# Kernel tuning notes

Hardware: AMD Instinct MI355X
Metric: run time of the kernel (lower is better)

## Reference

```python
import jax, jax.numpy as jnp
import numpy as np

EPS = 1e-3  # keras LayerNormalization default epsilon


def _layernorm(y, gamma, beta):
    m = jnp.mean(y, axis=-1, keepdims=True)
    v = jnp.var(y, axis=-1, keepdims=True)
    return (y - m) * jax.lax.rsqrt(v + EPS) * gamma + beta


def setup_inputs() -> dict:
    key = jax.random.key(0)
    ks = jax.random.split(key, 3)
    B, S, D, F = 4, 8192, 512, 2048
    x = jax.random.normal(ks[0], (B, S, D), dtype=jnp.float32)
    W1 = jax.random.normal(ks[1], (D, F), dtype=jnp.float32) * (1.0 / np.sqrt(D))
    b1 = jnp.zeros((F,), dtype=jnp.float32)
    W2 = jax.random.normal(ks[2], (F, D), dtype=jnp.float32) * (1.0 / np.sqrt(F))
    b2 = jnp.zeros((D,), dtype=jnp.float32)
    g1 = jnp.ones((D,), dtype=jnp.float32)
    be1 = jnp.zeros((D,), dtype=jnp.float32)
    g2 = jnp.ones((D,), dtype=jnp.float32)
    be2 = jnp.zeros((D,), dtype=jnp.float32)
    return {"x": x, "W1": W1, "b1": b1, "W2": W2, "b2": b2,
            "g1": g1, "be1": be1, "g2": g2, "be2": be2}


def reference(x, W1, b1, W2, b2, g1, be1, g2, be2):
    # 2D FFT over (seq, embed) axes; keep real part (FNet mixing)
    fft = jnp.real(jnp.fft.fft2(x.astype(jnp.complex64), axes=(-2, -1)))
    proj_input = _layernorm(x + fft, g1, be1)
    # FFN: Dense(dense_dim, relu) -> Dense(embed_dim)
    h = jax.nn.relu(jnp.einsum('bsd,df->bsf', proj_input, W1) + b1)
    proj_output = jnp.einsum('bsf,fd->bsd', h, W2) + b2
    return _layernorm(proj_input + proj_output, g2, be2)
```

## Files before the change

### kernel.cpp

```cpp
#include <hip/hip_runtime.h>

typedef unsigned short u16;
typedef unsigned int u32;
typedef short short8 __attribute__((ext_vector_type(8)));
typedef float f32x4 __attribute__((ext_vector_type(4)));

#define LN_EPS 1e-3f
#define PI2 6.28318530717958647692f
#define AS1 __attribute__((address_space(1)))
#define AS3 __attribute__((address_space(3)))

__device__ __forceinline__ u16 f2bf(float f) {
  u32 u = __float_as_uint(f);
  u += 0x7fffu + ((u >> 16) & 1u);
  return (u16)(u >> 16);
}
__device__ __forceinline__ float bf2f(u16 h) {
  return __uint_as_float(((u32)h) << 16);
}

__global__ __launch_bounds__(256) void prep_w(const float* __restrict__ W,
                                              u16* __restrict__ Wt, int R, int C) {
  __shared__ float tile[32][33];
  const int ct = C >> 5;
  int bc = blockIdx.x % ct;
  int br = blockIdx.x / ct;
  int tx = threadIdx.x & 31, ty = threadIdx.x >> 5;
  int r0 = br << 5, c0 = bc << 5;
#pragma unroll
  for (int i = 0; i < 32; i += 8)
    tile[ty + i][tx] = W[(size_t)(r0 + ty + i) * C + c0 + tx];
  __syncthreads();
#pragma unroll
  for (int i = 0; i < 32; i += 8)
    Wt[(size_t)(c0 + ty + i) * R + r0 + tx] = f2bf(tile[tx][ty + i]);
}

__global__ __launch_bounds__(256) void transpose_x(const float* __restrict__ x,
                                                   u16* __restrict__ xt) {
  __shared__ float tile[32][33];
  int blk = blockIdx.x;
  int b = blk >> 12;
  int rem = blk & 4095;
  int st = rem >> 4;
  int dt = rem & 15;
  int tx = threadIdx.x & 31, ty = threadIdx.x >> 5;
  int s0 = st << 5, d0 = dt << 5;
#pragma unroll
  for (int i = 0; i < 32; i += 8)
    tile[ty + i][tx] = x[(((size_t)(b << 13) + s0 + ty + i) << 9) + d0 + tx];
  __syncthreads();
#pragma unroll
  for (int i = 0; i < 32; i += 8)
    xt[(((size_t)(b << 9) + d0 + ty + i) << 13) + s0 + tx] = f2bf(tile[tx][ty + i]);
}

__device__ __constant__ float C16r[8] = {1.f, 0.92387953f, 0.70710678f, 0.38268343f,
                                         0.f, -0.38268343f, -0.70710678f, -0.92387953f};
__device__ __constant__ float C16i[8] = {0.f, -0.38268343f, -0.70710678f, -0.92387953f,
                                         -1.f, -0.92387953f, -0.70710678f, -0.38268343f};
__device__ __constant__ float C8r[4] = {1.f, 0.70710678f, 0.f, -0.70710678f};
__device__ __constant__ float C8i[4] = {0.f, -0.70710678f, -1.f, -0.70710678f};
__device__ __constant__ float C4r[2] = {1.f, 0.f};
__device__ __constant__ float C4i[2] = {0.f, -1.f};
__device__ __constant__ float C32r[16] = {
    1.f, 0.98078528f, 0.92387953f, 0.83146961f, 0.70710678f, 0.55557023f,
    0.38268343f, 0.19509032f, 0.f, -0.19509032f, -0.38268343f, -0.55557023f,
    -0.70710678f, -0.83146961f, -0.92387953f, -0.98078528f};
__device__ __constant__ float C32i[16] = {
    0.f, -0.19509032f, -0.38268343f, -0.55557023f, -0.70710678f, -0.83146961f,
    -0.92387953f, -0.98078528f, -1.f, -0.98078528f, -0.92387953f, -0.83146961f,
    -0.70710678f, -0.55557023f, -0.38268343f, -0.19509032f};
__device__ __constant__ int REV4[16] = {0, 8, 4, 12, 2, 10, 6, 14,
                                        1, 9, 5, 13, 3, 11, 7, 15};

__device__ __forceinline__ constexpr int rev4c(int v) {
  return ((v & 1) << 3) | ((v & 2) << 1) | ((v & 4) >> 1) | ((v & 8) >> 3);
}

#define BFLY(ar, ai, br, bi, wr, wi)                 \
  {                                                  \
    float dr_ = (ar) - (br), di_ = (ai) - (bi);      \
    (ar) += (br);                                    \
    (ai) += (bi);                                    \
    (br) = dr_ * (wr)-di_ * (wi);                    \
    (bi) = dr_ * (wi) + di_ * (wr);                  \
  }

__global__ __launch_bounds__(512) void fft_s(u16* __restrict__ X, u16* __restrict__ Xim) {
  __shared__ float zr[8448], zi[8448];
  const int t = threadIdx.x;
  const int b = blockIdx.x >> 8;
  const int d0 = (blockIdx.x & 255) << 1;
  u16* r0 = X + (((size_t)(b << 9) + d0) << 13);
  u16* r1 = r0 + 8192;

  float xr[16], xi[16];
#pragma unroll
  for (int e = 0; e < 16; ++e) {
    xr[e] = bf2f(r0[t + (e << 9)]);
    xi[e] = bf2f(r1[t + (e << 9)]);
  }

  float c1, s1;
  sincosf(-PI2 * (float)t * (1.0f / 8192.0f), &s1, &c1);
  float c2 = c1 * c1 - s1 * s1, s2 = 2.f * c1 * s1;
  float c4 = c2 * c2 - s2 * s2, s4 = 2.f * c2 * s2;
  float c8 = c4 * c4 - s4 * s4, s8 = 2.f * c4 * s4;
#pragma unroll
  for (int e = 0; e < 8; ++e) {
    float wr = c1 * C16r[e] - s1 * C16i[e];
    float wi = c1 * C16i[e] + s1 * C16r[e];
    BFLY(xr[e], xi[e], xr[e + 8], xi[e + 8], wr, wi);
  }
#pragma unroll
  for (int e = 0; e < 16; ++e) {
    if ((e & 4) == 0) {
      int eb = e & 3;
      float wr = c2 * C8r[eb] - s2 * C8i[eb];
      float wi = c2 * C8i[eb] + s2 * C8r[eb];
      BFLY(xr[e], xi[e], xr[e + 4], xi[e + 4], wr, wi);
    }
  }
#pragma unroll
  for (int e = 0; e < 16; ++e) {
    if (((e >> 1) & 1) == 0) {
      int eb = e & 1;
      float wr = c4 * C4r[eb] - s4 * C4i[eb];
      float wi = c4 * C4i[eb] + s4 * C4r[eb];
      BFLY(xr[e], xi[e], xr[e + 2], xi[e + 2], wr, wi);
    }
  }
#pragma unroll
  for (int e = 0; e < 16; e += 2) {
    BFLY(xr[e], xi[e], xr[e + 1], xi[e + 1], c8, s8);
  }

#pragma unroll
  for (int e = 0; e < 16; ++e) {
    int idx = t + (e << 9);
    int a = idx + (idx >> 5);
    zr[a] = xr[e];
    zi[a] = xi[e];
  }
  __syncthreads();
  {
    const int f = t >> 5, l = t & 31;
#pragma unroll
    for (int e = 0; e < 16; ++e) {
      int idx = (f << 9) + (e << 5) + l;
      int a = idx + (idx >> 5);
      xr[e] = zr[a];
      xi[e] = zi[a];
    }
    float bc1, bs1;
    sincosf(-PI2 * (float)l * (1.0f / 512.0f), &bs1, &bc1);
    float bc2 = bc1 * bc1 - bs1 * bs1, bs2 = 2.f * bc1 * bs1;
    float bc4 = bc2 * bc2 - bs2 * bs2, bs4 = 2.f * bc2 * bs2;
    float bc8 = bc4 * bc4 - bs4 * bs4, bs8 = 2.f * bc4 * bs4;
#pragma unroll
    for (int e = 0; e < 8; ++e) {
      float wr = bc1 * C16r[e] - bs1 * C16i[e];
      float wi = bc1 * C16i[e] + bs1 * C16r[e];
      BFLY(xr[e], xi[e], xr[e + 8], xi[e + 8], wr, wi);
    }
#pragma unroll
    for (int e = 0; e < 16; ++e) {
      if (((e >> 2) & 1) == 0) {
        int eb = e & 3;
        float wr = bc2 * C8r[eb] - bs2 * C8i[eb];
        float wi = bc2 * C8i[eb] + bs2 * C8r[eb];
        BFLY(xr[e], xi[e], xr[e + 4], xi[e + 4], wr, wi);
      }
    }
#pragma unroll
    for (int e = 0; e < 16; ++e) {
      if (((e >> 1) & 1) == 0) {
        int eb = e & 1;
        float wr = bc4 * C4r[eb] - bs4 * C4i[eb];
        float wi = bc4 * C4i[eb] + bs4 * C4r[eb];
        BFLY(xr[e], xi[e], xr[e + 2], xi[e + 2], wr, wi);
      }
    }
#pragma unroll
    for (int e = 0; e < 16; e += 2) {
      BFLY(xr[e], xi[e], xr[e + 1], xi[e + 1], bc8, bs8);
    }
    __syncthreads();
#pragma unroll
    for (int e = 0; e < 16; ++e) {
      int idx = (f << 9) + (e << 5) + l;
      int a = idx + (idx >> 5);
      zr[a] = xr[e];
      zi[a] = xi[e];
    }
  }
  __syncthreads();
#pragma unroll
  for (int j = 0; j < 16; ++j) {
    int idx = (t << 4) + j;
    int a = idx + (idx >> 5);
    xr[j] = zr[a];
    xi[j] = zi[a];
  }

  {
    const int odd = t & 1;
#pragma unroll
    for (int j = 0; j < 16; ++j) {
      float pr = __shfl_xor(xr[j], 1);
      float pi = __shfl_xor(xi[j], 1);
      if (!odd) {
        xr[j] += pr;
        xi[j] += pi;
      } else {
        float dr = pr - xr[j], di = pi - xi[j];
        xr[j] = dr * C32r[j] - di * C32i[j];
        xi[j] = dr * C32i[j] + di * C32r[j];
      }
    }
#pragma unroll
    for (int j = 0; j < 8; ++j) {
      BFLY(xr[j], xi[j], xr[j + 8], xi[j + 8], C16r[j], C16i[j]);
    }
#pragma unroll
    for (int j = 0; j < 16; ++j) {
      if (((j >> 2) & 1) == 0) {
        BFLY(xr[j], xi[j], xr[j + 4], xi[j + 4], C8r[j & 3], C8i[j & 3]);
      }
    }
#pragma unroll
    for (int j = 0; j < 16; ++j) {
      if (((j >> 1) & 1) == 0) {
        BFLY(xr[j], xi[j], xr[j + 2], xi[j + 2], C4r[j & 1], C4i[j & 1]);
      }
    }
#pragma unroll
    for (int j = 0; j < 16; j += 2) {
      BFLY(xr[j], xi[j], xr[j + 1], xi[j + 1], 1.0f, 0.0f);
    }
  }

  __syncthreads();
  {
    const int rt = __brev((u32)t) >> 23;
#pragma unroll
    for (int j = 0; j < 16; ++j) {
      int k = (REV4[j] << 9) | rt;
      int a = k + (k >> 5);
      zr[a] = xr[j];
      zi[a] = xi[j];
    }
  }
  __syncthreads();

  u16* i0 = Xim + (((size_t)(b << 9) + d0) << 13);
  u16* i1 = i0 + 8192;
#pragma unroll
  for (int e = 0; e < 8; ++e) {
    int k = t + (e << 9);
    int nk = (8192 - k) & 8191;
    int ka = k + (k >> 5), na = nk + (nk >> 5);
    float zrk = zr[ka], zik = zi[ka], zrn = zr[na], zin = zi[na];
    r0[k] = f2bf(0.5f * (zrk + zrn));
    i0[k] = f2bf(0.5f * (zik - zin));
    r1[k] = f2bf(0.5f * (zik + zin));
    i1[k] = f2bf(0.5f * (zrn - zrk));
  }
  if (t == 0) {
    const int ka = 4096 + (4096 >> 5);
    r0[4096] = f2bf(zr[ka]);
    i0[4096] = 0;
    r1[4096] = f2bf(zi[ka]);
    i1[4096] = 0;
  }
}

__global__ __launch_bounds__(256) void fft_d_ln(
    const u16* __restrict__ Xre, const u16* __restrict__ Xim,
    const float* __restrict__ x, const float* __restrict__ g1,
    const float* __restrict__ be1, u16* __restrict__ proj) {
  __shared__ float buf[16 * 528];
  const int tid = threadIdx.x;
  const int b = blockIdx.x / 257;
  const int kt = blockIdx.x - b * 257;
  const int s0 = kt << 4;
  const int row = tid >> 4, t = tid & 15;
  const int so = tid & 15, dd = tid >> 4;

  float xr[32], xi[32];

#pragma unroll
  for (int it = 0; it < 32; ++it) {
    int d = dd + (it << 4);
    buf[so * 516 + d] = bf2f(Xre[(((size_t)(b << 9) + d) << 13) + s0 + so]);
  }
  __syncthreads();
#pragma unroll
  for (int e = 0; e < 32; ++e) xr[e] = buf[row * 516 + t + (e << 4)];
  __syncthreads();
#pragma unroll
  for (int it = 0; it < 32; ++it) {
    int d = dd + (it << 4);
    buf[so * 516 + d] = bf2f(Xim[(((size_t)(b << 9) + d) << 13) + s0 + so]);
  }
  __syncthreads();
#pragma unroll
  for (int e = 0; e < 32; ++e) xi[e] = buf[row * 516 + t + (e << 4)];
  __syncthreads();

  float c1, s1;
  sincosf(-PI2 * (float)t * (1.0f / 512.0f), &s1, &c1);
  float c2 = c1 * c1 - s1 * s1, s2 = 2.f * c1 * s1;
  float c4 = c2 * c2 - s2 * s2, s4 = 2.f * c2 * s2;
  float c8 = c4 * c4 - s4 * s4, s8 = 2.f * c4 * s4;
  float c16 = c8 * c8 - s8 * s8, s16 = 2.f * c8 * s8;
#pragma unroll
  for (int e = 0; e < 16; ++e) {
    float wr = c1 * C32r[e] - s1 * C32i[e];
    float wi = c1 * C32i[e] + s1 * C32r[e];
    BFLY(xr[e], xi[e], xr[e + 16], xi[e + 16], wr, wi);
  }
#pragma unroll
  for (int e = 0; e < 32; ++e) {
    if ((e & 8) == 0) {
      int eb = e & 7;
      float wr = c2 * C16r[eb] - s2 * C16i[eb];
      float wi = c2 * C16i[eb] + s2 * C16r[eb];
      BFLY(xr[e], xi[e], xr[e + 8], xi[e + 8], wr, wi);
    }
  }
#pragma unroll
  for (int e = 0; e < 32; ++e) {
    if ((e & 4) == 0) {
      int eb = e & 3;
      float wr = c4 * C8r[eb] - s4 * C8i[eb];
      float wi = c4 * C8i[eb] + s4 * C8r[eb];
      BFLY(xr[e], xi[e], xr[e + 4], xi[e + 4], wr, wi);
    }
  }
#pragma unroll
  for (int e = 0; e < 32; ++e) {
    if ((e & 2) == 0) {
      int eb = e & 1;
      float wr = c8 * C4r[eb] - s8 * C4i[eb];
      float wi = c8 * C4i[eb] + s8 * C4r[eb];
      BFLY(xr[e], xi[e], xr[e + 2], xi[e + 2], wr, wi);
    }
  }
#pragma unroll
  for (int e = 0; e < 32; e += 2) {
    BFLY(xr[e], xi[e], xr[e + 1], xi[e + 1], c16, s16);
  }

#pragma unroll
  for (int e = 0; e < 32; ++e) {
    int p = (e << 4) + t;
    buf[row * 528 + p + (p >> 5)] = xr[e];
  }
  __syncthreads();
#pragma unroll
  for (int j = 0; j < 32; ++j) xr[j] = buf[row * 528 + 33 * t + j];
  __syncthreads();
#pragma unroll
  for (int e = 0; e < 32; ++e) {
    int p = (e << 4) + t;
    buf[row * 528 + p + (p >> 5)] = xi[e];
  }
  __syncthreads();
#pragma unroll
  for (int j = 0; j < 32; ++j) xi[j] = buf[row * 528 + 33 * t + j];
  __syncthreads();

#pragma unroll
  for (int o = 0; o < 32; o += 16) {
#pragma unroll
    for (int j = 0; j < 8; ++j)
      BFLY(xr[o + j], xi[o + j], xr[o + j + 8], xi[o + j + 8], C16r[j], C16i[j]);
#pragma unroll
    for (int j = 0; j < 16; ++j)
      if ((j & 4) == 0)
        BFLY(xr[o + j], xi[o + j], xr[o + j + 4], xi[o + j + 4], C8r[j & 3], C8i[j & 3]);
#pragma unroll
    for (int j = 0; j < 16; ++j)
      if ((j & 2) == 0)
        BFLY(xr[o + j], xi[o + j], xr[o + j + 2], xi[o + j + 2], C4r[j & 1], C4i[j & 1]);
#pragma unroll
    for (int j = 0; j < 16; j += 2)
      BFLY(xr[o + j], xi[o + j], xr[o + j + 1], xi[o + j + 1], 1.0f, 0.0f);
  }

  {
    const int rt4 = __brev((u32)t) >> 28;
#pragma unroll
    for (int j = 0; j < 16; ++j) {
      const int rj = rev4c(j);
      buf[row * 528 + 33 * rj + rt4] = xr[j];
      buf[row * 528 + 33 * rj + 16 + rt4] = xr[16 + j];
    }
  }
  __syncthreads();

  const int k = s0 + row;
  {
    const float* xrow = x + (((size_t)(b << 13) + k) << 9);
    float v[32];
    float sum = 0.f, sum2 = 0.f;
#pragma unroll
    for (int m = 0; m < 32; ++m) {
      int d = t + (m << 4);
      float val = buf[row * 528 + d + (d >> 5)] + xrow[d];
      v[m] = val;
      sum += val;
      sum2 += val * val;
    }
#pragma unroll
    for (int m = 1; m < 16; m <<= 1) {
      sum += __shfl_xor(sum, m, 16);
      sum2 += __shfl_xor(sum2, m, 16);
    }
    float mean = sum * (1.0f / 512.0f);
    float var = sum2 * (1.0f / 512.0f) - mean * mean;
    float scl = 1.0f / sqrtf(var + LN_EPS);
    if (k <= 4096) {
      u16* prow = proj + (((size_t)(b << 13) + k) << 9);
#pragma unroll
      for (int m = 0; m < 32; ++m) {
        int d = t + (m << 4);
        prow[d] = f2bf((v[m] - mean) * scl * g1[d] + be1[d]);
      }
    }
  }
  if (k >= 1 && k <= 4095) {
    const int sm = 8192 - k;
    const float* xrow = x + (((size_t)(b << 13) + sm) << 9);
    float v[32];
    float sum = 0.f, sum2 = 0.f;
#pragma unroll
    for (int m = 0; m < 32; ++m) {
      int d = t + (m << 4);
      int dm = (512 - d) & 511;
      float val = buf[row * 528 + dm + (dm >> 5)] + xrow[d];
      v[m] = val;
      sum += val;
      sum2 += val * val;
    }
#pragma unroll
    for (int m = 1; m < 16; m <<= 1) {
      sum += __shfl_xor(sum, m, 16);
      sum2 += __shfl_xor(sum2, m, 16);
    }
    float mean = sum * (1.0f / 512.0f);
    float var = sum2 * (1.0f / 512.0f) - mean * mean;
    float scl = 1.0f / sqrtf(var + LN_EPS);
    u16* prow = proj + (((size_t)(b << 13) + sm) << 9);
#pragma unroll
    for (int m = 0; m < 32; ++m) {
      int d = t + (m << 4);
      prow[d] = f2bf((v[m] - mean) * scl * g1[d] + be1[d]);
    }
  }
}

template <bool RELU, bool OUT_BF16, int GH>
__global__ __launch_bounds__(256, 2) void gemm_bt(
    const u16* __restrict__ A, const u16* __restrict__ Bt,
    const float* __restrict__ bias, void* __restrict__ Cout,
    int M, int N, int K) {
  const int tid = threadIdx.x;
  const int lane = tid & 63;
  const int wave = tid >> 6;
  const int wm = wave >> 1, wn = wave & 1;
  const int llo = lane & 15, lhi = lane >> 4;

  const int nwg = gridDim.x;
  const int q = nwg >> 3;
  const int b2 = ((int)blockIdx.x & 7) * q + ((int)blockIdx.x >> 3);
  const int NT = N >> 7;
  const int GSZ = GH * NT;
  const int grp = b2 / GSZ;
  const int r = b2 - grp * GSZ;
  const int tn = r / GH;
  const int tm = grp * GH + (r - tn * GH);
  const int m0 = tm << 7, n0 = tn << 7;

  __shared__ short8 smem[2048];
  char* ldsA = (char*)&smem[0];
  char* ldsB = ldsA + 16384;

  f32x4 acc[4][4] = {};

  const int trow = tid >> 3;
  const int ksw = (((tid & 7) ^ (trow & 7)) << 3);
  const int wbase = wave << 10;
  const int swz = (llo & 7) << 4;

  const int KT = K >> 6;
  for (int kt = 0; kt < KT; ++kt) {
    const int k0 = (kt << 6) + ksw;
    __syncthreads();
#pragma unroll
    for (int r4 = 0; r4 < 4; ++r4) {
      const int grow = (r4 << 5) + trow;
      const u16* ga = A + (size_t)(m0 + grow) * K + k0;
      const u16* gb = Bt + (size_t)(n0 + grow) * K + k0;
      __builtin_amdgcn_global_load_lds((const AS1 void*)ga,
                                       (AS3 void*)(ldsA + (r4 << 12) + wbase), 16, 0, 0);
      __builtin_amdgcn_global_load_lds((const AS1 void*)gb,
                                       (AS3 void*)(ldsB + (r4 << 12) + wbase), 16, 0, 0);
    }
    __syncthreads();
#pragma unroll
    for (int kk = 0; kk < 2; ++kk) {
      const int cbx = ((kk << 6) | (lhi << 4)) ^ swz;
      short8 af[4], bfr[4];
#pragma unroll
      for (int mt = 0; mt < 4; ++mt)
        af[mt] = *(const short8*)(ldsA + (((wm << 6) + (mt << 4) + llo) << 7) + cbx);
#pragma unroll
      for (int nt = 0; nt < 4; ++nt)
        bfr[nt] = *(const short8*)(ldsB + (((wn << 6) + (nt << 4) + llo) << 7) + cbx);
#pragma unroll
      for (int mt = 0; mt < 4; ++mt)
#pragma unroll
        for (int nt = 0; nt < 4; ++nt)
          acc[mt][nt] =
              __builtin_amdgcn_mfma_f32_16x16x32_bf16(af[mt], bfr[nt], acc[mt][nt], 0, 0, 0);
    }
  }
#pragma unroll
  for (int nt = 0; nt < 4; ++nt) {
    const int col = n0 + (wn << 6) + (nt << 4) + llo;
    const float bv = bias[col];
#pragma unroll
    for (int mt = 0; mt < 4; ++mt) {
      const int rbase = m0 + (wm << 6) + (mt << 4) + (lhi << 2);
#pragma unroll
      for (int j = 0; j < 4; ++j) {
        float v = acc[mt][nt][j] + bv;
        if (RELU) v = fmaxf(v, 0.0f);
        if (OUT_BF16) ((u16*)Cout)[(size_t)(rbase + j) * N + col] = f2bf(v);
        else          ((float*)Cout)[(size_t)(rbase + j) * N + col] = v;
      }
    }
  }
}

template <bool RELU, int OMODE, int GH>
__global__ __launch_bounds__(512, 2) void gemm256(
    const u16* __restrict__ A, const u16* __restrict__ Bt,
    const float* __restrict__ bias, void* __restrict__ Cout,
    int M, int N, int K) {
  const int tid = threadIdx.x;
  const int lane = tid & 63;
  const int wave = tid >> 6;
  const int wm = wave >> 2;
  const int wn = wave & 3;
  const int llo = lane & 15, lhi = lane >> 4;

  const int nwg = gridDim.x;
  const int q = nwg >> 3;
  const int b2 = ((int)blockIdx.x & 7) * q + ((int)blockIdx.x >> 3);
  const int NT = N >> 8;
  const int GSZ = GH * NT;
  const int grp = b2 / GSZ;
  const int rr = b2 - grp * GSZ;
  const int tn = rr / GH;
  const int tm = grp * GH + (rr - tn * GH);
  const int m0 = tm << 8, n0 = tn << 8;

  __shared__ short8 smem[8192];
  char* ldsA = (char*)&smem[0];
  char* ldsB = ldsA + 65536;

  f32x4 acc[8][4] = {};

  const int trow = tid >> 3;
  const int ksw = ((tid & 7) ^ (trow & 7)) << 3;
  const int swz = (llo & 7) << 4;
  const int cb0 = (lhi << 4) ^ swz;
  const char* Ab0 = ldsA + wm * 16384 + llo * 128;
  const char* Bb0 = ldsB + (wn >> 1) * 16384 + (((wn & 1) << 6) + llo) * 128;

#define GLDS(g_, d_) __builtin_amdgcn_global_load_lds((const AS1 void*)(g_), (AS3 void*)(d_), 16, 0, 0)
#define STAGE_A(kt, hf) {                                                        \
    const u16* g_ = A + (size_t)(m0 + ((hf) << 7) + trow) * K + ((kt) << 6) + ksw; \
    char* d_ = ldsA + (((kt)&1) << 15) + ((hf) << 14) + tid * 16;                \
    GLDS(g_, d_); GLDS(g_ + ((size_t)64) * K, d_ + 8192); }
#define STAGE_B(kt, hf) {                                                        \
    const u16* g_ = Bt + (size_t)(n0 + ((hf) << 7) + trow) * K + ((kt) << 6) + ksw; \
    char* d_ = ldsB + (((kt)&1) << 15) + ((hf) << 14) + tid * 16;                \
    GLDS(g_, d_); GLDS(g_ + ((size_t)64) * K, d_ + 8192); }
#define BAR() { __builtin_amdgcn_sched_barrier(0); __builtin_amdgcn_s_barrier(); \
                __builtin_amdgcn_sched_barrier(0); }
#define VMW(n_) { asm volatile("s_waitcnt vmcnt(" #n_ ")" ::: "memory"); }

  const int KT = K >> 6;
  STAGE_A(0, 0); STAGE_A(0, 1); STAGE_B(0, 0); STAGE_B(0, 1);
  STAGE_B(1, 0); STAGE_B(1, 1);
  VMW(0);
  BAR();

  for (int t0 = 0; t0 < KT; t0 += 2) {
    const bool pf = (t0 + 2 < KT);
#pragma unroll
    for (int s = 0; s < 2; ++s) {
      const char* Abase = Ab0 + (s << 15);
      const char* Bbase = Bb0 + (s << 15);
      short8 bfr[4][2];
      {
#pragma unroll
        for (int fn = 0; fn < 4; ++fn) {
          bfr[fn][0] = *(const short8*)(Bbase + fn * 2048 + cb0);
          bfr[fn][1] = *(const short8*)(Bbase + fn * 2048 + (cb0 ^ 64));
        }
        short8 af[2][2];
#pragma unroll
        for (int i = 0; i < 2; ++i) {
          af[i][0] = *(const short8*)(Abase + i * 2048 + cb0);
          af[i][1] = *(const short8*)(Abase + i * 2048 + (cb0 ^ 64));
        }
        if (s == 0) {
          STAGE_A(t0 + 1, 0); STAGE_A(t0 + 1, 1);
        } else if (pf) {
          STAGE_A(t0 + 2, 0); STAGE_A(t0 + 2, 1);
        }
        BAR();
        __builtin_amdgcn_s_setprio(1);
#pragma unroll
        for (int i = 0; i < 2; ++i)
#pragma unroll
          for (int fn = 0; fn < 4; ++fn)
#pragma unroll
            for (int kk = 0; kk < 2; ++kk)
              acc[i][fn] = __builtin_amdgcn_mfma_f32_16x16x32_bf16(
                  af[i][kk], bfr[fn][kk], acc[i][fn], 0, 0, 0);
        __builtin_amdgcn_s_setprio(0);
        BAR();
      }
#pragma unroll
      for (int qq = 1; qq < 4; ++qq) {
        short8 af[2][2];
#pragma unroll
        for (int i = 0; i < 2; ++i) {
          af[i][0] = *(const short8*)(Abase + (qq * 2 + i) * 2048 + cb0);
          af[i][1] = *(const short8*)(Abase + (qq * 2 + i) * 2048 + (cb0 ^ 64));
        }
        if (pf) {
          if (s == 0) {
            if (qq == 1) STAGE_B(t0 + 2, 0);
            if (qq == 2) STAGE_B(t0 + 2, 1);
          } else {
            if (qq == 1) STAGE_B(t0 + 3, 0);
            if (qq == 2) STAGE_B(t0 + 3, 1);
          }
        }
        BAR();
        __builtin_amdgcn_s_setprio(1);
#pragma unroll
        for (int i = 0; i < 2; ++i)
#pragma unroll
          for (int fn = 0; fn < 4; ++fn)
#pragma unroll
            for (int kk = 0; kk < 2; ++kk)
              acc[qq * 2 + i][fn] = __builtin_amdgcn_mfma_f32_16x16x32_bf16(
                  af[i][kk], bfr[fn][kk], acc[qq * 2 + i][fn], 0, 0, 0);
        __builtin_amdgcn_s_setprio(0);
        if (qq == 3) VMW(4);
        BAR();
      }
    }
  }
#undef GLDS
#undef STAGE_A
#undef STAGE_B
#undef BAR
#undef VMW

  float bv[4];
#pragma unroll
  for (int fn = 0; fn < 4; ++fn) bv[fn] = bias[n0 + (wn << 6) + (fn << 4) + llo];
#pragma unroll
  for (int fm = 0; fm < 8; ++fm) {
#pragma unroll
    for (int j = 0; j < 4; ++j) {
      const size_t row = (size_t)(m0 + (wm << 7) + (fm << 4) + (lhi << 2) + j);
#pragma unroll
      for (int fn = 0; fn < 4; ++fn) {
        const int col = n0 + (wn << 6) + (fn << 4) + llo;
        float v = acc[fm][fn][j] + bv[fn];
        if (RELU) v = fmaxf(v, 0.0f);
        if (OMODE == 2) {
          u16* P = (u16*)Cout;
          P[row * N + col] = f2bf(v + bf2f(P[row * N + col]));
        } else {
          ((u16*)Cout)[row * N + col] = f2bf(v);
        }
      }
    }
  }
}

__global__ __launch_bounds__(256) void ln2_kernel(
    float* __restrict__ out, const u16* __restrict__ y,
    const float* __restrict__ g2, const float* __restrict__ be2) {
  const int lane = threadIdx.x & 63;
  const int row = blockIdx.x * 4 + (threadIdx.x >> 6);
  const u16* yrow = y + ((size_t)row << 9);
  float* orow = out + ((size_t)row << 9);
  const int d0 = lane << 3;
  short8 p = *(const short8*)(yrow + d0);
  float yv[8];
  float sum = 0.f, sum2 = 0.f;
#pragma unroll
  for (int m = 0; m < 8; ++m) {
    float v = bf2f((u16)p[m]);
    yv[m] = v; sum += v; sum2 += v * v;
  }
#pragma unroll
  for (int m = 1; m < 64; m <<= 1) {
    sum += __shfl_xor(sum, m, 64);
    sum2 += __shfl_xor(sum2, m, 64);
  }
  float mean = sum * (1.0f / 512.0f);
  float var = sum2 * (1.0f / 512.0f) - mean * mean;
  float scl = 1.0f / sqrtf(var + LN_EPS);
  f32x4 g0 = *(const f32x4*)(g2 + d0);
  f32x4 g1v = *(const f32x4*)(g2 + d0 + 4);
  f32x4 e0 = *(const f32x4*)(be2 + d0);
  f32x4 e1 = *(const f32x4*)(be2 + d0 + 4);
  f32x4 o0, o1;
#pragma unroll
  for (int m = 0; m < 4; ++m) o0[m] = (yv[m] - mean) * scl * g0[m] + e0[m];
#pragma unroll
  for (int m = 0; m < 4; ++m) o1[m] = (yv[m + 4] - mean) * scl * g1v[m] + e1[m];
  *(f32x4*)(orow + d0) = o0;
  *(f32x4*)(orow + d0 + 4) = o1;
}

extern "C" void kernel_launch(void* const* d_in, const int* in_sizes, int n_in,
                              void* d_out, int out_size, void* d_ws, size_t ws_size,
                              hipStream_t stream) {
  const float* x   = (const float*)d_in[0];
  const float* W1  = (const float*)d_in[1];
  const float* b1  = (const float*)d_in[2];
  const float* W2  = (const float*)d_in[3];
  const float* b2  = (const float*)d_in[4];
  const float* g1  = (const float*)d_in[5];
  const float* be1 = (const float*)d_in[6];
  const float* g2  = (const float*)d_in[7];
  const float* be2 = (const float*)d_in[8];

  char* ws = (char*)d_ws;
  u16* xt   = (u16*)(ws);
  u16* xim  = (u16*)(ws + (32u << 20));
  u16* proj = (u16*)(ws + (128u << 20));
  u16* w1t  = (u16*)(ws + (160u << 20));
  u16* w2t  = (u16*)(ws + (162u << 20));
  u16* h    = (u16*)(ws);

  prep_w<<<1024, 256, 0, stream>>>(W1, w1t, 512, 2048);
  prep_w<<<1024, 256, 0, stream>>>(W2, w2t, 2048, 512);
  transpose_x<<<16384, 256, 0, stream>>>(x, xt);
  fft_s<<<1024, 512, 0, stream>>>(xt, xim);
  fft_d_ln<<<1028, 256, 0, stream>>>(xt, xim, x, g1, be1, proj);
  gemm_bt<true, true, 8><<<4096, 256, 0, stream>>>(proj, w1t, b1, (void*)h, 32768, 2048, 512);
  gemm256<false, 2, 2><<<256, 512, 0, stream>>>(h, w2t, b2, (void*)proj, 32768, 512, 2048);
  ln2_kernel<<<8192, 256, 0, stream>>>((float*)d_out, proj, g2, be2);
  (void)in_sizes; (void)n_in; (void)out_size; (void)ws_size;
}
```

Before: 266.5 us.

## Specialize first FFN GEMM for K=512 with full A tile in LDS and B in registers

Replaces the generic 128x128 tiled GEMM for the first FFN layer with a K=512-specialised kernel. It loads a full 64x512 A tile into LDS once (64 KB) and has each wave stream its B fragments directly from global memory into registers with double buffering, so the per-K-step LDS refill and its barriers go away. Tiles become 64x256 with one wave per 64 columns. The costs are 64 KB of LDS per block, which may limit occupancy, and uncached or poorly coalesced global loads for B that now bypass LDS.

```diff
diff --git a/kernel.cpp b/kernel.cpp
--- a/kernel.cpp
+++ b/kernel.cpp
@@ -462,85 +462,79 @@
   }
 }
 
-template <bool RELU, bool OUT_BF16, int GH>
-__global__ __launch_bounds__(256, 2) void gemm_bt(
+__global__ __launch_bounds__(256, 2) void gemm_k512(
     const u16* __restrict__ A, const u16* __restrict__ Bt,
-    const float* __restrict__ bias, void* __restrict__ Cout,
-    int M, int N, int K) {
+    const float* __restrict__ bias, u16* __restrict__ Cout, int N) {
   const int tid = threadIdx.x;
   const int lane = tid & 63;
   const int wave = tid >> 6;
-  const int wm = wave >> 1, wn = wave & 1;
   const int llo = lane & 15, lhi = lane >> 4;
 
   const int nwg = gridDim.x;
   const int q = nwg >> 3;
   const int b2 = ((int)blockIdx.x & 7) * q + ((int)blockIdx.x >> 3);
-  const int NT = N >> 7;
-  const int GSZ = GH * NT;
-  const int grp = b2 / GSZ;
-  const int r = b2 - grp * GSZ;
-  const int tn = r / GH;
-  const int tm = grp * GH + (r - tn * GH);
-  const int m0 = tm << 7, n0 = tn << 7;
-
-  __shared__ short8 smem[2048];
-  char* ldsA = (char*)&smem[0];
-  char* ldsB = ldsA + 16384;
+  const int tn = b2 & 7;
+  const int tm = b2 >> 3;
+  const int m0 = tm << 6, n0 = tn << 8;
+
+  __shared__ short8 smem[4096];
+  char* ldsA = (char*)smem;
+
+#pragma unroll
+  for (int i = 0; i < 16; ++i) {
+    const int r8 = (((i & 1) << 2) | (tid >> 6)) & 7;
+    const u16* g = A + (size_t)(m0 + (i << 2) + (tid >> 6)) * 512 +
+                   (((tid & 63) ^ r8) << 3);
+    __builtin_amdgcn_global_load_lds((const AS1 void*)g,
+                                     (AS3 void*)(ldsA + (i << 12) + tid * 16), 16, 0, 0);
+  }
+  __syncthreads();
 
   f32x4 acc[4][4] = {};
-
-  const int trow = tid >> 3;
-  const int ksw = (((tid & 7) ^ (trow & 7)) << 3);
-  const int wbase = wave << 10;
   const int swz = (llo & 7) << 4;
-
-  const int KT = K >> 6;
-  for (int kt = 0; kt < KT; ++kt) {
-    const int k0 = (kt << 6) + ksw;
-    __syncthreads();
-#pragma unroll
-    for (int r4 = 0; r4 < 4; ++r4) {
-      const int grow = (r4 << 5) + trow;
-      const u16* ga = A + (size_t)(m0 + grow) * K + k0;
-      const u16* gb = Bt + (size_t)(n0 + grow) * K + k0;
-      __builtin_amdgcn_global_load_lds((const AS1 void*)ga,
-                                       (AS3 void*)(ldsA + (r4 << 12) + wbase), 16, 0, 0);
-      __builtin_amdgcn_global_load_lds((const AS1 void*)gb,
-                                       (AS3 void*)(ldsB + (r4 << 12) + wbase), 16, 0, 0);
-    }
-    __syncthreads();
-#pragma unroll
-    for (int kk = 0; kk < 2; ++kk) {
-      const int cbx = ((kk << 6) | (lhi << 4)) ^ swz;
-      short8 af[4], bfr[4];
-#pragma unroll
-      for (int mt = 0; mt < 4; ++mt)
-        af[mt] = *(const short8*)(ldsA + (((wm << 6) + (mt << 4) + llo) << 7) + cbx);
-#pragma unroll
-      for (int nt = 0; nt < 4; ++nt)
-        bfr[nt] = *(const short8*)(ldsB + (((wn << 6) + (nt << 4) + llo) << 7) + cbx);
-#pragma unroll
-      for (int mt = 0; mt < 4; ++mt)
-#pragma unroll
-        for (int nt = 0; nt < 4; ++nt)
-          acc[mt][nt] =
-              __builtin_amdgcn_mfma_f32_16x16x32_bf16(af[mt], bfr[nt], acc[mt][nt], 0, 0, 0);
-    }
-  }
+  const u16* bp0 = Bt + (size_t)(n0 + (wave << 6) + llo) * 512 + (lhi << 3);
+
+#define LOADB(bb, s)                                                     \
+  {                                                                      \
+    _Pragma("unroll") for (int nt = 0; nt < 4; ++nt)                     \
+        bb[nt] = *(const short8*)(bp0 + (size_t)nt * 8192 + ((s) << 5)); \
+  }
+#define COMPUTE(bb, s)                                                              \
+  {                                                                                 \
+    short8 af[4];                                                                   \
+    _Pragma("unroll") for (int mt = 0; mt < 4; ++mt)                                \
+        af[mt] = *(const short8*)(ldsA + (((mt << 4) + llo) << 10) +                \
+                                  ((((s) << 6) + (lhi << 4)) ^ swz));               \
+    _Pragma("unroll") for (int mt = 0; mt < 4; ++mt)                                \
+        _Pragma("unroll") for (int nt = 0; nt < 4; ++nt)                            \
+            acc[mt][nt] = __builtin_amdgcn_mfma_f32_16x16x32_bf16(af[mt], bb[nt],   \
+                                                                  acc[mt][nt], 0, 0, 0); \
+  }
+
+  short8 b0[4], b1[4];
+  LOADB(b0, 0);
+  LOADB(b1, 1);
+#pragma unroll
+  for (int s2 = 0; s2 < 8; ++s2) {
+    COMPUTE(b0, 2 * s2);
+    if (s2 < 7) LOADB(b0, 2 * s2 + 2);
+    COMPUTE(b1, 2 * s2 + 1);
+    if (s2 < 7) LOADB(b1, 2 * s2 + 3);
+  }
+#undef LOADB
+#undef COMPUTE
+
 #pragma unroll
   for (int nt = 0; nt < 4; ++nt) {
-    const int col = n0 + (wn << 6) + (nt << 4) + llo;
+    const int col = n0 + (wave << 6) + (nt << 4) + llo;
     const float bv = bias[col];
 #pragma unroll
     for (int mt = 0; mt < 4; ++mt) {
-      const int rbase = m0 + (wm << 6) + (mt << 4) + (lhi << 2);
+      const int rbase = m0 + (mt << 4) + (lhi << 2);
 #pragma unroll
       for (int j = 0; j < 4; ++j) {
-        float v = acc[mt][nt][j] + bv;
-        if (RELU) v = fmaxf(v, 0.0f);
-        if (OUT_BF16) ((u16*)Cout)[(size_t)(rbase + j) * N + col] = f2bf(v);
-        else          ((float*)Cout)[(size_t)(rbase + j) * N + col] = v;
+        float v = fmaxf(acc[mt][nt][j] + bv, 0.0f);
+        Cout[(size_t)(rbase + j) * N + col] = f2bf(v);
       }
     }
   }
@@ -764,7 +758,7 @@
   transpose_x<<<16384, 256, 0, stream>>>(x, xt);
   fft_s<<<1024, 512, 0, stream>>>(xt, xim);
   fft_d_ln<<<1028, 256, 0, stream>>>(xt, xim, x, g1, be1, proj);
-  gemm_bt<true, true, 8><<<4096, 256, 0, stream>>>(proj, w1t, b1, (void*)h, 32768, 2048, 512);
+  gemm_k512<<<4096, 256, 0, stream>>>(proj, w1t, b1, h, 2048);
   gemm256<false, 2, 2><<<256, 512, 0, stream>>>(h, w2t, b2, (void*)proj, 32768, 512, 2048);
   ln2_kernel<<<8192, 256, 0, stream>>>((float*)d_out, proj, g2, be2);
   (void)in_sizes; (void)n_in; (void)out_size; (void)ws_size;
```

Result: slower. 318.9 us (+19.6%).
